# Kernel optimization log

Measured on AMD Instinct MI355X. Metric: run time of the kernel, lower is better.

Reference implementation:

```python
import jax, jax.numpy as jnp
import numpy as np

D_MODEL = 1024
N_HEADS = 16
MAX_SEQ = 1024
BATCH = 4

def _first_primes(n):
    limit = n * 15
    sieve = np.ones(limit, dtype=bool)
    sieve[:2] = False
    for i in range(2, int(limit ** 0.5) + 1):
        if sieve[i]:
            sieve[i * i::i] = False
    return np.flatnonzero(sieve)[:n]

def _pi_attention_bias(n_heads, max_seq_len):
    # bias[h, t, s] = 0.1 * sin(prime[h]*pi * (t - s) / max_seq_len)
    primes = _first_primes(n_heads).astype(np.float32)
    freqs = primes * np.pi  # [H]
    pos = np.arange(max_seq_len, dtype=np.float32)
    pos_diff = pos[:, None] - pos[None, :]  # [T, T]
    bias = np.sin(freqs[:, None, None] * pos_diff[None] / max_seq_len) * 0.1
    return jnp.asarray(bias, dtype=jnp.float32)

def setup_inputs() -> dict:
    key = jax.random.key(0)
    ks = jax.random.split(key, 8)
    D = D_MODEL
    xavier = (6.0 / (D + D)) ** 0.5
    inp = {
        'x': jax.random.normal(ks[0], (BATCH, MAX_SEQ, D), dtype=jnp.float32),
        'Wq': jax.random.uniform(ks[1], (D, D), jnp.float32, -xavier, xavier),
        'bq': jnp.zeros((D,), jnp.float32),
        'Wk': jax.random.uniform(ks[2], (D, D), jnp.float32, -xavier, xavier),
        'bk': jnp.zeros((D,), jnp.float32),
        'Wv': jax.random.uniform(ks[3], (D, D), jnp.float32, -xavier, xavier),
        'bv': jnp.zeros((D,), jnp.float32),
        'Wo': jax.random.uniform(ks[4], (D, D), jnp.float32, -xavier, xavier),
        'bo': jnp.zeros((D,), jnp.float32),
        'pi_bias': _pi_attention_bias(N_HEADS, MAX_SEQ),
        'bias_scale': jnp.asarray(0.1, jnp.float32),
        'spectral_alpha': jnp.asarray(1.0, jnp.float32),
    }
    return inp

def reference(x, Wq, bq, Wk, bk, Wv, bv, Wo, bo, pi_bias, bias_scale, spectral_alpha):
    B, T, D = x.shape
    H = N_HEADS
    hd = D // H
    scale = 1.0 / (hd ** 0.5)

    def split_heads(y):
        return y.reshape(B, T, H, hd).transpose(0, 2, 1, 3)  # [B,H,T,hd]

    q = split_heads(x @ Wq + bq)
    k = split_heads(x @ Wk + bk)
    v = split_heads(x @ Wv + bv)

    # spectral filter along the time axis (use_spectral and T > 4)
    freqs = jnp.fft.fftfreq(T).astype(jnp.float32)  # [T]
    filt = jnp.exp(-jnp.abs(spectral_alpha) * jnp.abs(freqs))[None, None, :, None]
    q = jnp.fft.ifft(jnp.fft.fft(q, axis=2, norm='ortho') * filt, axis=2, norm='ortho').real
    k = jnp.fft.ifft(jnp.fft.fft(k, axis=2, norm='ortho') * filt, axis=2, norm='ortho').real

    scores = jnp.einsum('bhtd,bhsd->bhts', q, k) * scale
    scores = scores + bias_scale * pi_bias[None, :, :T, :T]
    attn = jax.nn.softmax(scores, axis=-1)  # dropout is identity in eval
    out = jnp.einsum('bhts,bhsd->bhtd', attn, v)
    out = out.transpose(0, 2, 1, 3).reshape(B, T, D)
    return out @ Wo + bo
```

## Files before the change

### kernel.cpp

```cpp
#include <hip/hip_runtime.h>
#include <hip/hip_bf16.h>

typedef __bf16 bf16x8 __attribute__((ext_vector_type(8)));
typedef float f32x4 __attribute__((ext_vector_type(4)));
typedef unsigned short u16x8 __attribute__((ext_vector_type(8)));

#define OFF_G      0x0ULL
#define OFF_GMAT   0x10000ULL
#define OFF_XB     0x210000ULL
#define OFF_XBT    0xA10000ULL
#define OFF_XF     0x1210000ULL
#define OFF_WQT    0x1A10000ULL
#define OFF_WKT    0x1C10000ULL
#define OFF_WVT    0x1E10000ULL
#define OFF_WOT    0x2010000ULL
#define OFF_KB     0x2210000ULL
#define OFF_VTB    0x2A10000ULL

static __device__ __forceinline__ unsigned short f2bf(float f) {
  union { float f; unsigned int u; } v; v.f = f;
  unsigned int r = v.u + 0x7FFFu + ((v.u >> 16) & 1u);
  return (unsigned short)(r >> 16);
}

static __device__ __forceinline__ void g2l16(const unsigned short* g, unsigned short* l) {
  __builtin_amdgcn_global_load_lds(
      (const __attribute__((address_space(1))) unsigned int*)g,
      (__attribute__((address_space(3))) unsigned int*)l, 16, 0, 0);
}

__constant__ float PRIMES_F[16] = {2.f, 3.f, 5.f, 7.f, 11.f, 13.f, 17.f, 19.f,
                                   23.f, 29.f, 31.f, 37.f, 41.f, 43.f, 47.f, 53.f};

__global__ __launch_bounds__(256) void k_gmat(const float* __restrict__ g,
                                              unsigned short* __restrict__ Gm) {
  int i = (blockIdx.x * 256 + threadIdx.x) * 8;
  int t = i >> 10, s0 = i & 1023;
  u16x8 o;
  #pragma unroll
  for (int j = 0; j < 8; j++) o[j] = f2bf(g[(t - s0 - j) & 1023]);
  *(u16x8*)(&Gm[i]) = o;
}

__global__ __launch_bounds__(256) void k_prep(
    const float* __restrict__ x, const float* __restrict__ w0,
    const float* __restrict__ w1, const float* __restrict__ w2,
    const float* __restrict__ w3, const float* __restrict__ alpha_p,
    unsigned short* __restrict__ xb, unsigned short* __restrict__ xbT,
    unsigned short* __restrict__ Wout, float* __restrict__ g) {
  __shared__ float tile[32][33];
  __shared__ float red[4];
  const int z = blockIdx.z;
  if (z == 8) {
    const int d = blockIdx.y * 32 + blockIdx.x;
    const float alpha = fabsf(alpha_p[0]);
    float partial = 0.f;
    for (int j = threadIdx.x; j < 1024; j += 256) {
      int jm = (j <= 512) ? j : 1024 - j;
      float filt = __expf(-alpha * (float)jm * (1.0f / 1024.f));
      int p = (j * d) & 1023;
      partial += filt * __cosf((float)p * (6.28318530717958647692f / 1024.f));
    }
    #pragma unroll
    for (int off = 32; off > 0; off >>= 1) partial += __shfl_down(partial, off, 64);
    if ((threadIdx.x & 63) == 0) red[threadIdx.x >> 6] = partial;
    __syncthreads();
    if (threadIdx.x == 0) g[d] = (red[0] + red[1] + red[2] + red[3]) * (1.f / 1024.f);
    return;
  }
  const bool isX = z < 4;
  const float* in = isX ? (x + ((long)z << 20))
                        : (z == 4 ? w0 : z == 5 ? w1 : z == 6 ? w2 : w3);
  const long ooff = isX ? ((long)z << 20) : ((long)(z - 4) << 20);
  const int r0 = blockIdx.y * 32, c0 = blockIdx.x * 32;
  const int tx = threadIdx.x & 31, ty = threadIdx.x >> 5;
  #pragma unroll
  for (int i = 0; i < 4; i++) {
    float v = in[(long)(r0 + ty + 8 * i) * 1024 + c0 + tx];
    tile[ty + 8 * i][tx] = v;
    if (isX) xb[ooff + (long)(r0 + ty + 8 * i) * 1024 + c0 + tx] = f2bf(v);
  }
  __syncthreads();
  unsigned short* outT = isX ? xbT : Wout;
  #pragma unroll
  for (int i = 0; i < 4; i++)
    outT[ooff + (long)(c0 + ty + 8 * i) * 1024 + r0 + tx] = f2bf(tile[tx][ty + 8 * i]);
}

#define GEMM_CORE(A_, Bt_, ACC_)                                                     \
  const int tid = threadIdx.x, l = tid & 63, wid = tid >> 6;                         \
  const int lr = l & 15, lg = l >> 4;                                                \
  const int wm = (wid >> 1) * 64, wn = (wid & 1) * 64;                               \
  const int scol = ((l & 7) ^ (l >> 3)) * 8;                                         \
  const unsigned short* Ag = A_ + (long)(m0 + wid * 32 + (l >> 3)) * 1024 + scol;    \
  const unsigned short* Bg = Bt_ + (long)(n0 + wid * 32 + (l >> 3)) * 1024 + scol;   \
  const int xk = (lr & 7) << 4;                                                      \
  const int co[2] = {(0 + lg * 16) ^ xk, (64 + lg * 16) ^ xk};                       \
  {                                                                                  \
    _Pragma("unroll")                                                                \
    for (int c = 0; c < 4; c++) {                                                    \
      g2l16(Ag + (long)c * 8192, &As[0][wid * 2048 + c * 512]);                      \
      g2l16(Bg + (long)c * 8192, &Bs[0][wid * 2048 + c * 512]);                      \
    }                                                                                \
    Ag += 64; Bg += 64;                                                              \
  }                                                                                  \
  __syncthreads();                                                                   \
  for (int t = 0; t < 16; ++t) {                                                     \
    const int cur = t & 1;                                                           \
    if (t < 15) {                                                                    \
      const int nxt = cur ^ 1;                                                       \
      _Pragma("unroll")                                                              \
      for (int c = 0; c < 4; c++) {                                                  \
        g2l16(Ag + (long)c * 8192, &As[nxt][wid * 2048 + c * 512]);                  \
        g2l16(Bg + (long)c * 8192, &Bs[nxt][wid * 2048 + c * 512]);                  \
      }                                                                              \
      Ag += 64; Bg += 64;                                                            \
      asm volatile("s_waitcnt vmcnt(8)" ::: "memory");                               \
    } else {                                                                         \
      asm volatile("s_waitcnt vmcnt(0)" ::: "memory");                               \
    }                                                                                \
    __builtin_amdgcn_s_barrier();                                                    \
    __builtin_amdgcn_sched_barrier(0);                                               \
    const char* Ab = (const char*)&As[cur][0];                                       \
    const char* Bb = (const char*)&Bs[cur][0];                                       \
    _Pragma("unroll")                                                                \
    for (int ks = 0; ks < 2; ks++) {                                                 \
      bf16x8 af[4], bfr[4];                                                          \
      _Pragma("unroll")                                                              \
      for (int mf = 0; mf < 4; mf++)                                                 \
        af[mf] = *(const bf16x8*)(Ab + (wm + mf * 16 + lr) * 128 + co[ks]);          \
      _Pragma("unroll")                                                              \
      for (int nf = 0; nf < 4; nf++)                                                 \
        bfr[nf] = *(const bf16x8*)(Bb + (wn + nf * 16 + lr) * 128 + co[ks]);         \
      _Pragma("unroll")                                                              \
      for (int mf = 0; mf < 4; mf++)                                                 \
        _Pragma("unroll")                                                            \
        for (int nf = 0; nf < 4; nf++)                                               \
          ACC_[mf][nf] = __builtin_amdgcn_mfma_f32_16x16x32_bf16(af[mf], bfr[nf],    \
                                                                 ACC_[mf][nf], 0, 0, 0); \
    }                                                                                \
    __builtin_amdgcn_sched_barrier(0);                                               \
    __builtin_amdgcn_s_barrier();                                                    \
  }

__global__ __launch_bounds__(256) void k_gemm5(
    const unsigned short* __restrict__ A, const unsigned short* __restrict__ Bt,
    const float* __restrict__ bias, const float* __restrict__ bias2,
    unsigned short* __restrict__ Cv, unsigned short* __restrict__ Cv2) {
  __shared__ __align__(16) unsigned short As[2][128 * 64];
  __shared__ __align__(16) unsigned short Bs[2][128 * 64];
  const int orig = (blockIdx.x & 7) * 64 + (blockIdx.x >> 3);
  const int m0 = (orig & 31) * 128, n0 = (orig >> 5) * 128;
  f32x4 acc[4][4] = {};
  GEMM_CORE(A, Bt, acc)
  #pragma unroll
  for (int nf = 0; nf < 4; nf++) {
    const int n = n0 + wn + nf * 16 + lr;
    const float bb = (n < 1024) ? bias[n] : bias2[n - 1024];
    unsigned short* Cd = (n < 1024) ? Cv : Cv2;
    #pragma unroll
    for (int mf = 0; mf < 4; mf++) {
      const int mb = m0 + wm + mf * 16 + lg * 4;
      #pragma unroll
      for (int r = 0; r < 4; r++)
        Cd[(long)(mb + r) * 1024 + (n & 1023)] = f2bf(acc[mf][nf][r] + bb);
    }
  }
}

__global__ __launch_bounds__(256) void k_fv(
    const unsigned short* __restrict__ Gm, const unsigned short* __restrict__ xbT,
    const unsigned short* __restrict__ WvT, const unsigned short* __restrict__ xb,
    const float* __restrict__ bv, unsigned short* __restrict__ Xf,
    unsigned short* __restrict__ Vtb) {
  __shared__ __align__(16) unsigned short As[2][128 * 64];
  __shared__ __align__(16) unsigned short Bs[2][128 * 64];
  const int orig = (blockIdx.x & 7) * 64 + (blockIdx.x >> 3);
  const bool isV = orig >= 256;
  const int o = isV ? orig - 256 : orig;
  const int m0 = (o & 7) * 128, n0 = (o >> 3) * 128;
  const unsigned short* A_ = isV ? WvT : Gm;
  const unsigned short* Bt_ = isV ? xb : xbT;
  const int nk = isV ? 16 : 6;
  const int ktbase = isV ? 0 : ((m0 - 128) & 1023);
  const int tid = threadIdx.x, l = tid & 63, wid = tid >> 6;
  const int lr = l & 15, lg = l >> 4;
  const int wm = (wid >> 1) * 64, wn = (wid & 1) * 64;
  const int scol = ((l & 7) ^ (l >> 3)) * 8;
  const unsigned short* Ag = A_ + (long)(m0 + wid * 32 + (l >> 3)) * 1024 + scol;
  const unsigned short* Bg = Bt_ + (long)(n0 + wid * 32 + (l >> 3)) * 1024 + scol;
  const int xk = (lr & 7) << 4;
  const int co[2] = {(0 + lg * 16) ^ xk, (64 + lg * 16) ^ xk};
  {
    #pragma unroll
    for (int c = 0; c < 4; c++) {
      g2l16(Ag + (long)c * 8192 + ktbase, &As[0][wid * 2048 + c * 512]);
      g2l16(Bg + (long)c * 8192 + ktbase, &Bs[0][wid * 2048 + c * 512]);
    }
  }
  __syncthreads();
  f32x4 acc[4][4] = {};
  for (int t = 0; t < nk; ++t) {
    const int cur = t & 1;
    if (t < nk - 1) {
      const int nxt = cur ^ 1;
      const int kt = (ktbase + ((t + 1) << 6)) & 1023;
      #pragma unroll
      for (int c = 0; c < 4; c++) {
        g2l16(Ag + (long)c * 8192 + kt, &As[nxt][wid * 2048 + c * 512]);
        g2l16(Bg + (long)c * 8192 + kt, &Bs[nxt][wid * 2048 + c * 512]);
      }
      asm volatile("s_waitcnt vmcnt(8)" ::: "memory");
    } else {
      asm volatile("s_waitcnt vmcnt(0)" ::: "memory");
    }
    __builtin_amdgcn_s_barrier();
    __builtin_amdgcn_sched_barrier(0);
    const char* Ab = (const char*)&As[cur][0];
    const char* Bb = (const char*)&Bs[cur][0];
    #pragma unroll
    for (int ks = 0; ks < 2; ks++) {
      bf16x8 af[4], bfr[4];
      #pragma unroll
      for (int mf = 0; mf < 4; mf++)
        af[mf] = *(const bf16x8*)(Ab + (wm + mf * 16 + lr) * 128 + co[ks]);
      #pragma unroll
      for (int nf = 0; nf < 4; nf++)
        bfr[nf] = *(const bf16x8*)(Bb + (wn + nf * 16 + lr) * 128 + co[ks]);
      #pragma unroll
      for (int mf = 0; mf < 4; mf++)
        #pragma unroll
        for (int nf = 0; nf < 4; nf++)
          acc[mf][nf] = __builtin_amdgcn_mfma_f32_16x16x32_bf16(af[mf], bfr[nf], acc[mf][nf], 0, 0, 0);
    }
    __builtin_amdgcn_sched_barrier(0);
    __builtin_amdgcn_s_barrier();
  }
  #pragma unroll
  for (int nf = 0; nf < 4; nf++) {
    const int n = n0 + wn + nf * 16 + lr;
    #pragma unroll
    for (int mf = 0; mf < 4; mf++) {
      const int mb = wm + mf * 16 + lg * 4;
      #pragma unroll
      for (int r = 0; r < 4; r++) {
        const int m = m0 + mb + r;
        float v = acc[mf][nf][r];
        if (isV) {
          Vtb[(long)m * 4096 + n] = f2bf(v + bv[m]);
        } else {
          Xf[(long)((n & ~1023) + m) * 1024 + (n & 1023)] = f2bf(v);
        }
      }
    }
  }
}

__global__ __launch_bounds__(256) void k_gemmO(
    const unsigned short* __restrict__ A, const unsigned short* __restrict__ Bt,
    const float* __restrict__ bias, float* __restrict__ C) {
  __shared__ __align__(16) unsigned short As[2][64 * 64];
  __shared__ __align__(16) unsigned short Bs[2][128 * 64];
  const int orig = (blockIdx.x & 7) * 64 + (blockIdx.x >> 3);
  const int m0 = (orig & 63) * 64, n0 = (orig >> 6) * 128;
  const int tid = threadIdx.x, l = tid & 63, wid = tid >> 6;
  const int lr = l & 15, lg = l >> 4;
  const int wm = (wid >> 1) * 32, wn = (wid & 1) * 64;
  const int scol = ((l & 7) ^ (l >> 3)) * 8;
  const unsigned short* Ag = A + (long)(m0 + wid * 16 + (l >> 3)) * 1024 + scol;
  const unsigned short* Bg = Bt + (long)(n0 + wid * 32 + (l >> 3)) * 1024 + scol;
  const int xk = (lr & 7) << 4;
  const int co[2] = {(0 + lg * 16) ^ xk, (64 + lg * 16) ^ xk};
  {
    #pragma unroll
    for (int c = 0; c < 2; c++) g2l16(Ag + (long)c * 8192, &As[0][wid * 1024 + c * 512]);
    #pragma unroll
    for (int c = 0; c < 4; c++) g2l16(Bg + (long)c * 8192, &Bs[0][wid * 2048 + c * 512]);
    Ag += 64; Bg += 64;
  }
  __syncthreads();
  f32x4 acc[2][4] = {};
  for (int t = 0; t < 16; ++t) {
    const int cur = t & 1;
    if (t < 15) {
      const int nxt = cur ^ 1;
      #pragma unroll
      for (int c = 0; c < 2; c++) g2l16(Ag + (long)c * 8192, &As[nxt][wid * 1024 + c * 512]);
      #pragma unroll
      for (int c = 0; c < 4; c++) g2l16(Bg + (long)c * 8192, &Bs[nxt][wid * 2048 + c * 512]);
      Ag += 64; Bg += 64;
      asm volatile("s_waitcnt vmcnt(6)" ::: "memory");
    } else {
      asm volatile("s_waitcnt vmcnt(0)" ::: "memory");
    }
    __builtin_amdgcn_s_barrier();
    __builtin_amdgcn_sched_barrier(0);
    const char* Ab = (const char*)&As[cur][0];
    const char* Bb = (const char*)&Bs[cur][0];
    #pragma unroll
    for (int ks = 0; ks < 2; ks++) {
      bf16x8 af[2], bfr[4];
      #pragma unroll
      for (int mf = 0; mf < 2; mf++)
        af[mf] = *(const bf16x8*)(Ab + (wm + mf * 16 + lr) * 128 + co[ks]);
      #pragma unroll
      for (int nf = 0; nf < 4; nf++)
        bfr[nf] = *(const bf16x8*)(Bb + (wn + nf * 16 + lr) * 128 + co[ks]);
      #pragma unroll
      for (int mf = 0; mf < 2; mf++)
        #pragma unroll
        for (int nf = 0; nf < 4; nf++)
          acc[mf][nf] = __builtin_amdgcn_mfma_f32_16x16x32_bf16(af[mf], bfr[nf], acc[mf][nf], 0, 0, 0);
    }
    __builtin_amdgcn_sched_barrier(0);
    __builtin_amdgcn_s_barrier();
  }
  #pragma unroll
  for (int nf = 0; nf < 4; nf++) {
    const int n = n0 + wn + nf * 16 + lr;
    const float bb = bias[n];
    #pragma unroll
    for (int mf = 0; mf < 2; mf++) {
      const int mb = m0 + wm + mf * 16 + lg * 4;
      #pragma unroll
      for (int r = 0; r < 4; r++)
        C[(long)(mb + r) * 1024 + n] = acc[mf][nf][r] + bb;
    }
  }
}

__global__ __launch_bounds__(512) void k_attn(
    const unsigned short* __restrict__ Qb, const unsigned short* __restrict__ Kb,
    const unsigned short* __restrict__ Vtb,
    const float* __restrict__ bias_scale_p, unsigned short* __restrict__ Ob) {
  __shared__ __align__(16) unsigned short Kbuf[3][4096];
  __shared__ __align__(16) unsigned short Vbuf[3][4096];
  __shared__ __align__(16) unsigned short Ps[8][16 * 64];
  const int bid = blockIdx.x;
  const int qt = (bid >> 3) & 7;
  const int hb = ((bid >> 6) << 3) | (bid & 7);
  const int h = hb & 15, b = hb >> 4;
  const int tid = threadIdx.x, l = tid & 63, wid = tid >> 6;
  const int lr = l & 15, lg = l >> 4;
  const int q0 = qt * 128;
  const float LOG2E = 1.44269504088896f;
  const float c10 = bias_scale_p[0] * 0.1f * LOG2E;
  const float k1 = 0.125f * LOG2E;
  const float fh = PRIMES_F[h] * 3.14159265358979323846f;
  const unsigned short* Vth = Vtb + (long)h * 64 * 4096 + b * 1024;
  const int xk = (lr & 7) << 4;
  const int co[2] = {(0 + lg * 16) ^ xk, (64 + lg * 16) ^ xk};
  const int scol = ((l & 7) ^ (l >> 3)) * 8;

  const unsigned short* kg = Kb + (long)(b * 1024 + wid * 8 + (l >> 3)) * 1024 + h * 64 + scol;
  const unsigned short* vg = Vth + (long)(wid * 8 + (l >> 3)) * 4096 + scol;
  unsigned short* kls = &Kbuf[0][0];
  unsigned short* vls = &Vbuf[0][0];
  #define STAGE_TO(BI) \
    { g2l16(kg, kls + (BI) * 4096 + wid * 512); \
      g2l16(vg, vls + (BI) * 4096 + wid * 512); \
      kg += 64 * 1024; vg += 64; }

  STAGE_TO(0);
  STAGE_TO(1);

  bf16x8 af[2];
  #pragma unroll
  for (int ks = 0; ks < 2; ks++)
    af[ks] = *(const bf16x8*)(
        &Qb[(long)(b * 1024 + q0 + wid * 16 + lr) * 1024 + h * 64 + ks * 32 + lg * 8]);

  float st2[4], ct2[4];
  #pragma unroll
  for (int r = 0; r < 4; r++) {
    float tt = (float)(q0 + wid * 16 + lg * 4 + r);
    float s_, c_;
    __sincosf(fh * tt * (1.f / 1024.f), &s_, &c_);
    st2[r] = c10 * s_;
    ct2[r] = c10 * c_;
  }
  float ss4[4], cs4[4], sd, cd;
  __sincosf(fh * (1.f / 16.f), &sd, &cd);
  #pragma unroll
  for (int nf = 0; nf < 4; nf++)
    __sincosf(fh * (float)(nf * 16 + lr) * (1.f / 1024.f), &ss4[nf], &cs4[nf]);

  f32x4 acc_o[4] = {};
  float pden[4] = {};
  int cur = 0, stg = 2;
  __syncthreads();

  for (int it = 0; it < 16; ++it) {
    if (it < 15) {
      asm volatile("s_waitcnt vmcnt(2)" ::: "memory");
    } else {
      asm volatile("s_waitcnt vmcnt(0)" ::: "memory");
    }
    __builtin_amdgcn_s_barrier();
    __builtin_amdgcn_sched_barrier(0);
    if (it < 14) { STAGE_TO(stg); }
    const char* Kbb = (const char*)kls + cur * 8192;
    const char* Vbb = (const char*)vls + cur * 8192;
    f32x4 accs[4] = {};
    #pragma unroll
    for (int ks = 0; ks < 2; ks++) {
      bf16x8 bfr[4];
      #pragma unroll
      for (int nf = 0; nf < 4; nf++)
        bfr[nf] = *(const bf16x8*)(Kbb + (nf * 16 + lr) * 128 + co[ks]);
      __builtin_amdgcn_s_setprio(1);
      #pragma unroll
      for (int nf = 0; nf < 4; nf++)
        accs[nf] = __builtin_amdgcn_mfma_f32_16x16x32_bf16(af[ks], bfr[nf], accs[nf], 0, 0, 0);
      __builtin_amdgcn_s_setprio(0);
    }
    char* Pw = (char*)&Ps[wid][0];
    #pragma unroll
    for (int nf = 0; nf < 4; nf++) {
      #pragma unroll
      for (int r = 0; r < 4; r++) {
        float v = fmaf(accs[nf][r], k1, fmaf(st2[r], cs4[nf], -ct2[r] * ss4[nf]));
        float p;
        asm("v_exp_f32 %0, %1" : "=v"(p) : "v"(v));
        pden[r] += p;
        union { float f; unsigned int u; } pu; pu.f = p;
        const int prow = lg * 4 + r;
        *(unsigned short*)(Pw + prow * 128 + ((nf * 32 + lr * 2) ^ ((prow & 7) << 4))) =
            (unsigned short)((pu.u + 0x8000u) >> 16);
      }
    }
    #pragma unroll
    for (int ks = 0; ks < 2; ks++) {
      bf16x8 pa = *(const bf16x8*)(Pw + lr * 128 + co[ks]);
      bf16x8 vb[4];
      #pragma unroll
      for (int nf = 0; nf < 4; nf++)
        vb[nf] = *(const bf16x8*)(Vbb + (nf * 16 + lr) * 128 + co[ks]);
      __builtin_amdgcn_s_setprio(1);
      #pragma unroll
      for (int nf = 0; nf < 4; nf++)
        acc_o[nf] = __builtin_amdgcn_mfma_f32_16x16x32_bf16(pa, vb[nf], acc_o[nf], 0, 0, 0);
      __builtin_amdgcn_s_setprio(0);
    }
    #pragma unroll
    for (int nf = 0; nf < 4; nf++) {
      float c_ = cs4[nf] * cd - ss4[nf] * sd;
      ss4[nf] = ss4[nf] * cd + cs4[nf] * sd;
      cs4[nf] = c_;
    }
    cur = (cur == 2) ? 0 : cur + 1;
    stg = (stg == 2) ? 0 : stg + 1;
  }
  #undef STAGE_TO
  #pragma unroll
  for (int r = 0; r < 4; r++) {
    float dsum = pden[r];
    #pragma unroll
    for (int off = 1; off < 16; off <<= 1) dsum += __shfl_xor(dsum, off, 64);
    pden[r] = 1.0f / dsum;
  }
  const int tg = q0 + wid * 16 + lg * 4;
  #pragma unroll
  for (int nf = 0; nf < 4; nf++) {
    const int dd = nf * 16 + lr;
    #pragma unroll
    for (int r = 0; r < 4; r++) {
      float val = acc_o[nf][r] * pden[r];
      Ob[(long)(b * 1024 + tg + r) * 1024 + h * 64 + dd] = f2bf(val);
    }
  }
}

extern "C" void kernel_launch(void* const* d_in, const int* in_sizes, int n_in,
                              void* d_out, int out_size, void* d_ws, size_t ws_size,
                              hipStream_t stream) {
  const float* x   = (const float*)d_in[0];
  const float* Wq  = (const float*)d_in[1];
  const float* bq  = (const float*)d_in[2];
  const float* Wk  = (const float*)d_in[3];
  const float* bk  = (const float*)d_in[4];
  const float* Wv  = (const float*)d_in[5];
  const float* bv  = (const float*)d_in[6];
  const float* Wo  = (const float*)d_in[7];
  const float* bo  = (const float*)d_in[8];
  const float* bsc = (const float*)d_in[10];
  const float* alp = (const float*)d_in[11];
  char* ws = (char*)d_ws;
  float*          g   = (float*)(ws + OFF_G);
  unsigned short* Gm  = (unsigned short*)(ws + OFF_GMAT);
  unsigned short* xb  = (unsigned short*)(ws + OFF_XB);
  unsigned short* xbT = (unsigned short*)(ws + OFF_XBT);
  unsigned short* Xf  = (unsigned short*)(ws + OFF_XF);
  unsigned short* WqT = (unsigned short*)(ws + OFF_WQT);
  unsigned short* WvT = (unsigned short*)(ws + OFF_WVT);
  unsigned short* WoT = (unsigned short*)(ws + OFF_WOT);
  unsigned short* Qb  = xbT;
  unsigned short* Kb  = (unsigned short*)(ws + OFF_KB);
  unsigned short* Vtb = (unsigned short*)(ws + OFF_VTB);
  unsigned short* Ob  = Xf;

  k_prep<<<dim3(32, 32, 9), 256, 0, stream>>>(x, Wq, Wk, Wv, Wo, alp, xb, xbT, WqT, g);
  k_gmat<<<512, 256, 0, stream>>>(g, Gm);
  k_fv<<<512, 256, 0, stream>>>(Gm, xbT, WvT, xb, bv, Xf, Vtb);
  k_gemm5<<<512, 256, 0, stream>>>(Xf, WqT, bq, bk, Qb, Kb);
  k_attn<<<512, 512, 0, stream>>>(Qb, Kb, Vtb, bsc, Ob);
  k_gemmO<<<512, 256, 0, stream>>>(Ob, WoT, bo, (float*)d_out);
}
```

Before: 123.2 us.

## Compute circulant filter matrix in closed form inside prep, drop gmat kernel

Replaces the per-entry 1024-term cosine sum and the separate kernel that expanded it into a bf16 circulant matrix with a geometric-series closed form. Each Gm entry is now written straight from the z==8 slice of the prep kernel. This removes one kernel launch and its dependency, and cuts the O(N) reduction per lag to O(1). The fv kernel's block-to-tile mapping is also changed so V blocks come first with a different swizzle. The closed form relies on an alpha clamp and a division that could lose precision for small alpha.

```diff
diff --git a/kernel.cpp b/kernel.cpp
--- a/kernel.cpp
+++ b/kernel.cpp
@@ -3,9 +3,7 @@
 
 typedef __bf16 bf16x8 __attribute__((ext_vector_type(8)));
 typedef float f32x4 __attribute__((ext_vector_type(4)));
-typedef unsigned short u16x8 __attribute__((ext_vector_type(8)));
-
-#define OFF_G      0x0ULL
+
 #define OFF_GMAT   0x10000ULL
 #define OFF_XB     0x210000ULL
 #define OFF_XBT    0xA10000ULL
@@ -32,48 +30,39 @@
 __constant__ float PRIMES_F[16] = {2.f, 3.f, 5.f, 7.f, 11.f, 13.f, 17.f, 19.f,
                                    23.f, 29.f, 31.f, 37.f, 41.f, 43.f, 47.f, 53.f};
 
-__global__ __launch_bounds__(256) void k_gmat(const float* __restrict__ g,
-                                              unsigned short* __restrict__ Gm) {
-  int i = (blockIdx.x * 256 + threadIdx.x) * 8;
-  int t = i >> 10, s0 = i & 1023;
-  u16x8 o;
-  #pragma unroll
-  for (int j = 0; j < 8; j++) o[j] = f2bf(g[(t - s0 - j) & 1023]);
-  *(u16x8*)(&Gm[i]) = o;
-}
-
 __global__ __launch_bounds__(256) void k_prep(
     const float* __restrict__ x, const float* __restrict__ w0,
     const float* __restrict__ w1, const float* __restrict__ w2,
     const float* __restrict__ w3, const float* __restrict__ alpha_p,
     unsigned short* __restrict__ xb, unsigned short* __restrict__ xbT,
-    unsigned short* __restrict__ Wout, float* __restrict__ g) {
+    unsigned short* __restrict__ Wout, unsigned short* __restrict__ Gm) {
   __shared__ float tile[32][33];
-  __shared__ float red[4];
   const int z = blockIdx.z;
+  const int r0 = blockIdx.y * 32, c0 = blockIdx.x * 32;
+  const int tx = threadIdx.x & 31, ty = threadIdx.x >> 5;
   if (z == 8) {
-    const int d = blockIdx.y * 32 + blockIdx.x;
-    const float alpha = fabsf(alpha_p[0]);
-    float partial = 0.f;
-    for (int j = threadIdx.x; j < 1024; j += 256) {
-      int jm = (j <= 512) ? j : 1024 - j;
-      float filt = __expf(-alpha * (float)jm * (1.0f / 1024.f));
-      int p = (j * d) & 1023;
-      partial += filt * __cosf((float)p * (6.28318530717958647692f / 1024.f));
-    }
-    #pragma unroll
-    for (int off = 32; off > 0; off >>= 1) partial += __shfl_down(partial, off, 64);
-    if ((threadIdx.x & 63) == 0) red[threadIdx.x >> 6] = partial;
-    __syncthreads();
-    if (threadIdx.x == 0) g[d] = (red[0] + red[1] + red[2] + red[3]) * (1.f / 1024.f);
+    const float alpha = fmaxf(fabsf(alpha_p[0]), 1e-6f);
+    const float q = __expf(-alpha * (1.f / 1024.f));
+    const float q512 = __expf(-alpha * 0.5f);
+    #pragma unroll
+    for (int i = 0; i < 4; i++) {
+      const int t = r0 + ty + 8 * i, s = c0 + tx;
+      const int d = (t - s) & 1023;
+      float s_, c_;
+      __sincosf((float)d * (6.28318530717958647692f / 1024.f), &s_, &c_);
+      const float sgn = (d & 1) ? -1.f : 1.f;
+      const float Nr = q * c_ - q512 * sgn, Ni = q * s_;
+      const float Wr = 1.f - q * c_, Wi = -q * s_;
+      const float sum = (Nr * Wr + Ni * Wi) / (Wr * Wr + Wi * Wi);
+      const float gd = (1.f + q512 * sgn + 2.f * sum) * (1.f / 1024.f);
+      Gm[(long)t * 1024 + s] = f2bf(gd);
+    }
     return;
   }
   const bool isX = z < 4;
   const float* in = isX ? (x + ((long)z << 20))
                         : (z == 4 ? w0 : z == 5 ? w1 : z == 6 ? w2 : w3);
   const long ooff = isX ? ((long)z << 20) : ((long)(z - 4) << 20);
-  const int r0 = blockIdx.y * 32, c0 = blockIdx.x * 32;
-  const int tx = threadIdx.x & 31, ty = threadIdx.x >> 5;
   #pragma unroll
   for (int i = 0; i < 4; i++) {
     float v = in[(long)(r0 + ty + 8 * i) * 1024 + c0 + tx];
@@ -175,9 +164,9 @@
     unsigned short* __restrict__ Vtb) {
   __shared__ __align__(16) unsigned short As[2][128 * 64];
   __shared__ __align__(16) unsigned short Bs[2][128 * 64];
-  const int orig = (blockIdx.x & 7) * 64 + (blockIdx.x >> 3);
-  const bool isV = orig >= 256;
-  const int o = isV ? orig - 256 : orig;
+  const bool isV = blockIdx.x < 256;
+  const int inner = blockIdx.x & 255;
+  const int o = (inner & 7) * 32 + (inner >> 3);
   const int m0 = (o & 7) * 128, n0 = (o >> 3) * 128;
   const unsigned short* A_ = isV ? WvT : Gm;
   const unsigned short* Bt_ = isV ? xb : xbT;
@@ -486,7 +475,6 @@
   const float* bsc = (const float*)d_in[10];
   const float* alp = (const float*)d_in[11];
   char* ws = (char*)d_ws;
-  float*          g   = (float*)(ws + OFF_G);
   unsigned short* Gm  = (unsigned short*)(ws + OFF_GMAT);
   unsigned short* xb  = (unsigned short*)(ws + OFF_XB);
   unsigned short* xbT = (unsigned short*)(ws + OFF_XBT);
@@ -499,8 +487,7 @@
   unsigned short* Vtb = (unsigned short*)(ws + OFF_VTB);
   unsigned short* Ob  = Xf;
 
-  k_prep<<<dim3(32, 32, 9), 256, 0, stream>>>(x, Wq, Wk, Wv, Wo, alp, xb, xbT, WqT, g);
-  k_gmat<<<512, 256, 0, stream>>>(g, Gm);
+  k_prep<<<dim3(32, 32, 9), 256, 0, stream>>>(x, Wq, Wk, Wv, Wo, alp, xb, xbT, WqT, Gm);
   k_fv<<<512, 256, 0, stream>>>(Gm, xbT, WvT, xb, bv, Xf, Vtb);
   k_gemm5<<<512, 256, 0, stream>>>(Xf, WqT, bq, bk, Qb, Kb);
   k_attn<<<512, 512, 0, stream>>>(Qb, Kb, Vtb, bsc, Ob);
```

Result: faster. 117.8 us (-4.4%).
